# Optimization experiments

Hardware: AMD Instinct MI355X
Metric: run time of the kernel (lower is better)

The kernel has to match this reference:

```python
import jax, jax.numpy as jnp
import numpy as np

MAX_WORDS = 2048  # max word tokens per sequence (static num_segments)


def setup_inputs() -> dict:
    key = jax.random.key(0)
    k1, k2, k3, k4 = jax.random.split(key, 4)
    B, S, H, D = 8, 4096, 768, 1024
    embeddings = jax.random.normal(k1, (B, S, H), dtype=jnp.float32)
    proj_w = jax.random.normal(k2, (H, D), dtype=jnp.float32) * 0.02
    proj_b = jax.random.normal(k3, (D,), dtype=jnp.float32) * 0.02
    masks = jnp.ones((B, S), dtype=jnp.int32)
    word_ids = jnp.sort(jax.random.randint(k4, (B, S), 0, MAX_WORDS), axis=-1)
    return {"embeddings": embeddings, "proj_w": proj_w, "proj_b": proj_b,
            "masks": masks, "word_ids": word_ids}


def reference(embeddings, proj_w, proj_b, masks, word_ids):
    B, S, H = embeddings.shape
    W = MAX_WORDS
    # Flatten batch+word into one segment id space: seg in [0, B*W)
    seg = (word_ids + jnp.arange(B, dtype=word_ids.dtype)[:, None] * W).reshape(-1)
    flat_emb = embeddings.reshape(B * S, H)
    # segment-sum of embeddings over subwords of each word  -> (B, W, H)
    sum_emb = jax.ops.segment_sum(flat_emb, seg, num_segments=B * W).reshape(B, W, H)
    ones = jnp.ones((B * S,), dtype=jnp.float32)
    counts = jax.ops.segment_sum(ones, seg, num_segments=B * W).reshape(B, W)
    mcounts = jax.ops.segment_sum(masks.reshape(-1).astype(jnp.float32), seg,
                                  num_segments=B * W).reshape(B, W)
    # word is valid iff it has >=1 subword and ALL its subwords have mask==1
    valid = (counts > 0) & (counts == mcounts)
    mean_emb = sum_emb / jnp.maximum(counts, 1.0)[..., None]
    token_embeddings = jnp.where(valid[..., None], mean_emb, 0.0)  # (B, W, H)
    token_masks = valid.astype(jnp.int32)                          # (B, W)
    # projection: hidden 768 -> config.hidden_size 1024
    out = jnp.einsum('bwh,hd->bwd', token_embeddings, proj_w) + proj_b
    return out, token_masks
```

## Files before the change

### kernel.cpp

```cpp
#include <hip/hip_runtime.h>
#include <hip/hip_bf16.h>
#include <stdint.h>

#define Bn 8
#define Sn 4096
#define Hn 768
#define Dn 1024
#define Wn 2048

typedef __attribute__((ext_vector_type(8))) short short8;
typedef __attribute__((ext_vector_type(4))) short short4v;
typedef __attribute__((ext_vector_type(4))) float floatx4;

__device__ __forceinline__ void load_lds16(const void* g, void* l) {
  __builtin_amdgcn_global_load_lds(
      (const __attribute__((address_space(1))) void*)g,
      (__attribute__((address_space(3))) void*)l, 16, 0, 0);
}

__device__ __forceinline__ int lb4096(const int* __restrict__ a, int x, int lane) {
  const int p = a[lane << 6];
  const unsigned long long m1 = __ballot(p < x);
  const int n1 = __popcll(m1);
  const int base = (n1 > 0 ? n1 - 1 : 0) << 6;
  const int q = a[base + lane];
  const unsigned long long m2 = __ballot(q < x);
  return base + __popcll(m2);
}

__global__ __launch_bounds__(256) void k_front(const float* __restrict__ emb,
                                               const float* __restrict__ pw,
                                               const int* __restrict__ masks,
                                               const int* __restrict__ wid,
                                               __hip_bfloat16* __restrict__ wb,
                                               __hip_bfloat16* __restrict__ wa,
                                               float* __restrict__ out_masks) {
  const int bid = blockIdx.x;
  if (bid < 768) {
    __shared__ float tile[32][33];
    const int bt = bid;
    const int d0 = (bt % 32) * 32, h0 = (bt / 32) * 32;
    const int tx = threadIdx.x & 31, ty = threadIdx.x >> 5;
#pragma unroll
    for (int i = 0; i < 32; i += 8)
      tile[ty + i][tx] = pw[(size_t)(h0 + ty + i) * Dn + d0 + tx];
    __syncthreads();
#pragma unroll
    for (int i = 0; i < 32; i += 8)
      wb[(size_t)(d0 + ty + i) * Hn + h0 + tx] = (__hip_bfloat16)tile[tx][ty + i];
    return;
  }

  const int wbid = bid - 768;
  const int b = wbid >> 9;
  const int wave = threadIdx.x >> 6, lane = threadIdx.x & 63;
  const int w = (wbid & 511) * 4 + wave;

  const int* wbi = wid + (size_t)b * Sn;
  const int start = lb4096(wbi, w, lane);
  const int end = lb4096(wbi, w + 1, lane);
  const int count = end - start;

  const int* mb = masks + (size_t)b * Sn;
  bool allone = true;
  for (int s0 = start; s0 < end; s0 += 64) {
    const int idx = s0 + lane;
    allone = allone && ((idx < end) ? (mb[idx] == 1) : true);
  }
  const bool valid = (count > 0) && __all(allone);
  const float inv = valid ? 1.0f / (float)count : 0.0f;

  floatx4 sum[3] = {{0.f, 0.f, 0.f, 0.f}, {0.f, 0.f, 0.f, 0.f}, {0.f, 0.f, 0.f, 0.f}};
  const float* eb = emb + (size_t)b * Sn * Hn;
  int s = start;
  for (; s + 1 < end; s += 2) {
    const floatx4* r0 = (const floatx4*)(eb + (size_t)s * Hn);
    const floatx4* r1 = (const floatx4*)(eb + (size_t)(s + 1) * Hn);
#pragma unroll
    for (int j = 0; j < 3; ++j) sum[j] += r0[j * 64 + lane];
#pragma unroll
    for (int j = 0; j < 3; ++j) sum[j] += r1[j * 64 + lane];
  }
  if (s < end) {
    const floatx4* r0 = (const floatx4*)(eb + (size_t)s * Hn);
#pragma unroll
    for (int j = 0; j < 3; ++j) sum[j] += r0[j * 64 + lane];
  }

  const size_t rowbase = ((size_t)b * Wn + w) * Hn;
#pragma unroll
  for (int j = 0; j < 3; ++j) {
    short4v o;
#pragma unroll
    for (int c = 0; c < 4; ++c) {
      __hip_bfloat16 h = (__hip_bfloat16)(sum[j][c] * inv);
      o[c] = *reinterpret_cast<short*>(&h);
    }
    *(short4v*)&wa[rowbase + (size_t)(j * 64 + lane) * 4] = o;
  }
  if (lane == 0) out_masks[(size_t)b * Wn + w] = valid ? 1.0f : 0.0f;
}

constexpr int GK = Hn;
constexpr int TS = 256 * 64;
constexpr int kGemmLds = 2 * 2 * TS * (int)sizeof(short);
static_assert(kGemmLds == 131072, "LDS budget");

__global__ __launch_bounds__(512, 2) void k_gemm(const short* __restrict__ A,
                                                 const short* __restrict__ Bt,
                                                 const float* __restrict__ bias,
                                                 float* __restrict__ out) {
  extern __shared__ __align__(16) short ls[];

  const int t = threadIdx.x;
  const int lane = t & 63, wave = t >> 6;
  const int wm = wave >> 2, wn = wave & 3;
  const int lane16 = lane & 15, quad = lane >> 4;
  const int swz = lane16 & 7;

  const int mt = blockIdx.x & 63, nt = blockIdx.x >> 6;
  const int m0 = mt * 256, n0 = nt * 256;

  const int rS = t >> 3;
  const int csw = ((t & 7) ^ (rS & 7)) * 8;
  const short* gAs = A + (size_t)(m0 + rS) * GK + csw;
  const short* gBs = Bt + (size_t)(n0 + rS) * GK + csw;
  const int dst0 = t * 8;

  auto stage_a = [&](int buf, int kt) {
    short* d = ls + buf * 2 * TS + dst0;
    const short* g = gAs + kt * 64;
#pragma unroll
    for (int j = 0; j < 4; ++j) load_lds16(g + (size_t)(j * 64) * GK, d + j * 4096);
  };
  auto stage_b = [&](int buf, int kt) {
    short* d = ls + buf * 2 * TS + TS + dst0;
    const short* g = gBs + kt * 64;
#pragma unroll
    for (int j = 0; j < 4; ++j) load_lds16(g + (size_t)(j * 64) * GK, d + j * 4096);
  };

  auto ld_a = [&](short8(&af)[4][2], int qm, const short* bufA) {
#pragma unroll
    for (int mf = 0; mf < 4; ++mf)
#pragma unroll
      for (int ks = 0; ks < 2; ++ks)
        af[mf][ks] = *(const short8*)&bufA[(wm * 128 + qm * 64 + mf * 16 + lane16) * 64 +
                                           ((((ks << 2) | quad) ^ swz) << 3)];
  };
  auto ld_b = [&](short8(&bf)[2][2], int qn, const short* bufB) {
#pragma unroll
    for (int nf = 0; nf < 2; ++nf)
#pragma unroll
      for (int ks = 0; ks < 2; ++ks)
        bf[nf][ks] = *(const short8*)&bufB[(wn * 64 + qn * 32 + nf * 16 + lane16) * 64 +
                                           ((((ks << 2) | quad) ^ swz) << 3)];
  };

  floatx4 acc[8][4];
#pragma unroll
  for (int i = 0; i < 8; ++i)
#pragma unroll
    for (int j = 0; j < 4; ++j) acc[i][j] = (floatx4){0.f, 0.f, 0.f, 0.f};

  auto mm = [&](short8(&af)[4][2], short8(&bf)[2][2], int qm, int qn) {
    __builtin_amdgcn_s_setprio(1);
#pragma unroll
    for (int mf = 0; mf < 4; ++mf)
#pragma unroll
      for (int nf = 0; nf < 2; ++nf)
#pragma unroll
        for (int ks = 0; ks < 2; ++ks)
          acc[qm * 4 + mf][qn * 2 + nf] = __builtin_amdgcn_mfma_f32_16x16x32_bf16(
              af[mf][ks], bf[nf][ks], acc[qm * 4 + mf][qn * 2 + nf], 0, 0, 0);
    __builtin_amdgcn_s_setprio(0);
  };

  float bv[4];
#pragma unroll
  for (int nf = 0; nf < 4; ++nf) bv[nf] = bias[n0 + wn * 64 + nf * 16 + lane16];

  auto store_quad = [&](int qm, int qn) {
#pragma unroll
    for (int mf = 0; mf < 4; ++mf) {
#pragma unroll
      for (int nf = 0; nf < 2; ++nf) {
        const int n = n0 + wn * 64 + (qn * 2 + nf) * 16 + lane16;
#pragma unroll
        for (int r = 0; r < 4; ++r) {
          const int m = m0 + wm * 128 + (qm * 4 + mf) * 16 + quad * 4 + r;
          __builtin_nontemporal_store(acc[qm * 4 + mf][qn * 2 + nf][r] + bv[qn * 2 + nf],
                                      &out[(size_t)m * Dn + n]);
        }
      }
    }
  };

  stage_a(0, 0);
  stage_b(0, 0);
  __syncthreads();

#pragma unroll 1
  for (int kt = 0; kt < 11; ++kt) {
    const short* bufA = ls + (kt & 1) * 2 * TS;
    const short* bufB = bufA + TS;
    const int nb = (kt + 1) & 1;
    short8 af[4][2], b0[2][2], b1[2][2];

    ld_a(af, 0, bufA);
    ld_b(b0, 0, bufB);
    stage_a(nb, kt + 1);
    mm(af, b0, 0, 0);

    ld_b(b1, 1, bufB);
    stage_b(nb, kt + 1);
    mm(af, b1, 0, 1);

    ld_a(af, 1, bufA);
    mm(af, b1, 1, 1);

    mm(af, b0, 1, 0);

    __syncthreads();
  }

  {
    const short* bufA = ls + (11 & 1) * 2 * TS;
    const short* bufB = bufA + TS;
    short8 af[4][2], b0[2][2], b1[2][2];

    ld_a(af, 0, bufA);
    ld_b(b0, 0, bufB);
    mm(af, b0, 0, 0);
    store_quad(0, 0);

    ld_b(b1, 1, bufB);
    mm(af, b1, 0, 1);
    store_quad(0, 1);

    ld_a(af, 1, bufA);
    mm(af, b1, 1, 1);
    store_quad(1, 1);

    mm(af, b0, 1, 0);
    store_quad(1, 0);
  }
}

extern "C" void kernel_launch(void* const* d_in, const int* in_sizes, int n_in,
                              void* d_out, int out_size, void* d_ws, size_t ws_size,
                              hipStream_t stream) {
  const float* emb    = (const float*)d_in[0];
  const float* proj_w = (const float*)d_in[1];
  const float* proj_b = (const float*)d_in[2];
  const int*   masks  = (const int*)d_in[3];
  const int*   wid    = (const int*)d_in[4];

  float* out = (float*)d_out;
  float* out_masks = out + (size_t)Bn * Wn * Dn;

  __hip_bfloat16* wb = (__hip_bfloat16*)d_ws;
  __hip_bfloat16* wa = wb + (size_t)Dn * Hn;

  k_front<<<dim3(768 + 4096), 256, 0, stream>>>(emb, proj_w, masks, wid, wb, wa,
                                                out_masks);

  (void)hipFuncSetAttribute((const void*)k_gemm,
                            hipFuncAttributeMaxDynamicSharedMemorySize, kGemmLds);
  k_gemm<<<dim3(256), 512, kGemmLds, stream>>>((const short*)wa, (const short*)wb,
                                               proj_b, out);
}
```

Before: 204.4 us.

## Restructure GEMM into 4-stage K=32 LDS pipeline with explicit waitcnt barriers

The bf16 GEMM main loop changes from a double-buffered K=64 tile into a four-slot ring of K=32 tiles, prefetching three stages ahead. It uses raw s_barrier plus hand-placed vmcnt/lgkmcnt waits instead of __syncthreads, and the LDS swizzle shrinks to 4 chunks. The aim is to hide global-to-LDS latency more deeply and sync less conservatively, at the cost of more loop iterations and barriers, and a fragile hand-counted wait scheme.

```diff
diff --git a/kernel.cpp b/kernel.cpp
--- a/kernel.cpp
+++ b/kernel.cpp
@@ -102,8 +102,9 @@
 }
 
 constexpr int GK = Hn;
-constexpr int TS = 256 * 64;
-constexpr int kGemmLds = 2 * 2 * TS * (int)sizeof(short);
+constexpr int TSA = 256 * 32;
+constexpr int SLOT = 2 * TSA;
+constexpr int kGemmLds = 4 * SLOT * (int)sizeof(short);
 static_assert(kGemmLds == 131072, "LDS budget");
 
 __global__ __launch_bounds__(512, 2) void k_gemm(const short* __restrict__ A,
@@ -116,45 +117,41 @@
   const int lane = t & 63, wave = t >> 6;
   const int wm = wave >> 2, wn = wave & 3;
   const int lane16 = lane & 15, quad = lane >> 4;
-  const int swz = lane16 & 7;
+  const int swz2 = lane16 & 3;
 
   const int mt = blockIdx.x & 63, nt = blockIdx.x >> 6;
   const int m0 = mt * 256, n0 = nt * 256;
 
-  const int rS = t >> 3;
-  const int csw = ((t & 7) ^ (rS & 7)) * 8;
+  const int rS = t >> 2;
+  const int csw = ((t & 3) ^ (rS & 3)) * 8;
   const short* gAs = A + (size_t)(m0 + rS) * GK + csw;
   const short* gBs = Bt + (size_t)(n0 + rS) * GK + csw;
   const int dst0 = t * 8;
 
-  auto stage_a = [&](int buf, int kt) {
-    short* d = ls + buf * 2 * TS + dst0;
-    const short* g = gAs + kt * 64;
-#pragma unroll
-    for (int j = 0; j < 4; ++j) load_lds16(g + (size_t)(j * 64) * GK, d + j * 4096);
-  };
-  auto stage_b = [&](int buf, int kt) {
-    short* d = ls + buf * 2 * TS + TS + dst0;
-    const short* g = gBs + kt * 64;
-#pragma unroll
-    for (int j = 0; j < 4; ++j) load_lds16(g + (size_t)(j * 64) * GK, d + j * 4096);
-  };
-
-  auto ld_a = [&](short8(&af)[4][2], int qm, const short* bufA) {
+  auto stage_a = [&](int slot, int kt) {
+    short* d = ls + slot * SLOT + dst0;
+    const short* g = gAs + kt * 32;
+    load_lds16(g, d);
+    load_lds16(g + (size_t)128 * GK, d + 4096);
+  };
+  auto stage_b = [&](int slot, int kt) {
+    short* d = ls + slot * SLOT + TSA + dst0;
+    const short* g = gBs + kt * 32;
+    load_lds16(g, d);
+    load_lds16(g + (size_t)128 * GK, d + 4096);
+  };
+
+  auto ld_a = [&](short8(&af)[4], int mh, const short* bufA) {
 #pragma unroll
     for (int mf = 0; mf < 4; ++mf)
-#pragma unroll
-      for (int ks = 0; ks < 2; ++ks)
-        af[mf][ks] = *(const short8*)&bufA[(wm * 128 + qm * 64 + mf * 16 + lane16) * 64 +
-                                           ((((ks << 2) | quad) ^ swz) << 3)];
-  };
-  auto ld_b = [&](short8(&bf)[2][2], int qn, const short* bufB) {
-#pragma unroll
-    for (int nf = 0; nf < 2; ++nf)
-#pragma unroll
-      for (int ks = 0; ks < 2; ++ks)
-        bf[nf][ks] = *(const short8*)&bufB[(wn * 64 + qn * 32 + nf * 16 + lane16) * 64 +
-                                           ((((ks << 2) | quad) ^ swz) << 3)];
+      af[mf] = *(const short8*)&bufA[(wm * 128 + mh * 64 + mf * 16 + lane16) * 32 +
+                                     ((quad ^ swz2) << 3)];
+  };
+  auto ld_b = [&](short8(&bf)[4], const short* bufB) {
+#pragma unroll
+    for (int nf = 0; nf < 4; ++nf)
+      bf[nf] = *(const short8*)&bufB[(wn * 64 + nf * 16 + lane16) * 32 +
+                                     ((quad ^ swz2) << 3)];
   };
 
   floatx4 acc[8][4];
@@ -163,87 +160,95 @@
 #pragma unroll
     for (int j = 0; j < 4; ++j) acc[i][j] = (floatx4){0.f, 0.f, 0.f, 0.f};
 
-  auto mm = [&](short8(&af)[4][2], short8(&bf)[2][2], int qm, int qn) {
+  auto mm = [&](short8(&af)[4], short8(&bf)[4], int mh) {
     __builtin_amdgcn_s_setprio(1);
 #pragma unroll
     for (int mf = 0; mf < 4; ++mf)
 #pragma unroll
-      for (int nf = 0; nf < 2; ++nf)
-#pragma unroll
-        for (int ks = 0; ks < 2; ++ks)
-          acc[qm * 4 + mf][qn * 2 + nf] = __builtin_amdgcn_mfma_f32_16x16x32_bf16(
-              af[mf][ks], bf[nf][ks], acc[qm * 4 + mf][qn * 2 + nf], 0, 0, 0);
+      for (int nf = 0; nf < 4; ++nf)
+        acc[mh * 4 + mf][nf] = __builtin_amdgcn_mfma_f32_16x16x32_bf16(
+            af[mf], bf[nf], acc[mh * 4 + mf][nf], 0, 0, 0);
     __builtin_amdgcn_s_setprio(0);
   };
 
-  float bv[4];
-#pragma unroll
-  for (int nf = 0; nf < 4; ++nf) bv[nf] = bias[n0 + wn * 64 + nf * 16 + lane16];
-
-  auto store_quad = [&](int qm, int qn) {
-#pragma unroll
-    for (int mf = 0; mf < 4; ++mf) {
-#pragma unroll
-      for (int nf = 0; nf < 2; ++nf) {
-        const int n = n0 + wn * 64 + (qn * 2 + nf) * 16 + lane16;
-#pragma unroll
-        for (int r = 0; r < 4; ++r) {
-          const int m = m0 + wm * 128 + (qm * 4 + mf) * 16 + quad * 4 + r;
-          __builtin_nontemporal_store(acc[qm * 4 + mf][qn * 2 + nf][r] + bv[qn * 2 + nf],
-                                      &out[(size_t)m * Dn + n]);
+  stage_a(0, 0); stage_b(0, 0);
+  stage_a(1, 1); stage_b(1, 1);
+  stage_a(2, 2); stage_b(2, 2);
+  asm volatile("s_waitcnt vmcnt(8)" ::: "memory");
+  __builtin_amdgcn_sched_barrier(0);
+  __builtin_amdgcn_s_barrier();
+
+#pragma unroll 1
+  for (int kt = 0; kt < 23; ++kt) {
+    const short* bufA = ls + (kt & 3) * SLOT;
+    const short* bufB = bufA + TSA;
+    const int ss = (kt + 3) & 3;
+    const bool st = (kt <= 20);
+    short8 af[4], bf[4];
+
+    ld_a(af, 0, bufA);
+    ld_b(bf, bufB);
+    if (st) stage_a(ss, kt + 3);
+    __builtin_amdgcn_s_barrier();
+    asm volatile("s_waitcnt lgkmcnt(0)" ::: "memory");
+    __builtin_amdgcn_sched_barrier(0);
+    mm(af, bf, 0);
+    __builtin_amdgcn_s_barrier();
+
+    ld_a(af, 1, bufA);
+    if (st) stage_b(ss, kt + 3);
+    __builtin_amdgcn_s_barrier();
+    asm volatile("s_waitcnt lgkmcnt(0)" ::: "memory");
+    __builtin_amdgcn_sched_barrier(0);
+    mm(af, bf, 1);
+    if (kt <= 20) {
+      asm volatile("s_waitcnt vmcnt(8)" ::: "memory");
+    } else if (kt == 21) {
+      asm volatile("s_waitcnt vmcnt(4)" ::: "memory");
+    } else {
+      asm volatile("s_waitcnt vmcnt(0)" ::: "memory");
+    }
+    __builtin_amdgcn_sched_barrier(0);
+    __builtin_amdgcn_s_barrier();
+  }
+
+  {
+    const short* bufA = ls + 3 * SLOT;
+    const short* bufB = bufA + TSA;
+    short8 af[4], bf[4];
+
+    float bv[4];
+#pragma unroll
+    for (int nf = 0; nf < 4; ++nf) bv[nf] = bias[n0 + wn * 64 + nf * 16 + lane16];
+
+    auto store_half = [&](int mh) {
+#pragma unroll
+      for (int mf = 0; mf < 4; ++mf) {
+#pragma unroll
+        for (int nf = 0; nf < 4; ++nf) {
+          const int n = n0 + wn * 64 + nf * 16 + lane16;
+#pragma unroll
+          for (int r = 0; r < 4; ++r) {
+            const int m = m0 + wm * 128 + (mh * 4 + mf) * 16 + quad * 4 + r;
+            __builtin_nontemporal_store(acc[mh * 4 + mf][nf][r] + bv[nf],
+                                        &out[(size_t)m * Dn + n]);
+          }
         }
       }
-    }
-  };
-
-  stage_a(0, 0);
-  stage_b(0, 0);
-  __syncthreads();
-
-#pragma unroll 1
-  for (int kt = 0; kt < 11; ++kt) {
-    const short* bufA = ls + (kt & 1) * 2 * TS;
-    const short* bufB = bufA + TS;
-    const int nb = (kt + 1) & 1;
-    short8 af[4][2], b0[2][2], b1[2][2];
+    };
 
     ld_a(af, 0, bufA);
-    ld_b(b0, 0, bufB);
-    stage_a(nb, kt + 1);
-    mm(af, b0, 0, 0);
-
-    ld_b(b1, 1, bufB);
-    stage_b(nb, kt + 1);
-    mm(af, b1, 0, 1);
+    ld_b(bf, bufB);
+    asm volatile("s_waitcnt lgkmcnt(0)" ::: "memory");
+    __builtin_amdgcn_sched_barrier(0);
+    mm(af, bf, 0);
+    store_half(0);
 
     ld_a(af, 1, bufA);
-    mm(af, b1, 1, 1);
-
-    mm(af, b0, 1, 0);
-
-    __syncthreads();
-  }
-
-  {
-    const short* bufA = ls + (11 & 1) * 2 * TS;
-    const short* bufB = bufA + TS;
-    short8 af[4][2], b0[2][2], b1[2][2];
-
-    ld_a(af, 0, bufA);
-    ld_b(b0, 0, bufB);
-    mm(af, b0, 0, 0);
-    store_quad(0, 0);
-
-    ld_b(b1, 1, bufB);
-    mm(af, b1, 0, 1);
-    store_quad(0, 1);
-
-    ld_a(af, 1, bufA);
-    mm(af, b1, 1, 1);
-    store_quad(1, 1);
-
-    mm(af, b0, 1, 0);
-    store_quad(1, 0);
+    asm volatile("s_waitcnt lgkmcnt(0)" ::: "memory");
+    __builtin_amdgcn_sched_barrier(0);
+    mm(af, bf, 1);
+    store_half(1);
   }
 }
 
```

Result: slower. 210.6 us (+3.0%).
